# Kernel optimization log

Hardware: AMD Instinct MI355X
Metric: run time of the kernel (lower is better)

Reference implementation:

```python
import jax, jax.numpy as jnp
from jax import lax
import numpy as np

EPS = 1e-5
STRIDE = 4
K_NEIGHBORS = 16


def setup_inputs() -> dict:
    key = jax.random.key(0)
    ks = jax.random.split(key, 4)
    B, N, Cin, Cout = 16, 4096, 64, 128
    p1 = jax.random.normal(ks[0], (B, N, 3), dtype=jnp.float32)
    x1 = jax.random.normal(ks[1], (B, Cin, N), dtype=jnp.float32)
    w1 = jax.random.normal(ks[2], (Cout, Cin + 3), dtype=jnp.float32) * 0.05
    w2 = jax.random.normal(ks[3], (Cout, Cout), dtype=jnp.float32) * 0.05
    g1 = jnp.ones((Cout,), jnp.float32)
    b1 = jnp.zeros((Cout,), jnp.float32)
    g2 = jnp.ones((Cout,), jnp.float32)
    b2 = jnp.zeros((Cout,), jnp.float32)
    return {"p1": p1, "x1": x1, "w1": w1, "g1": g1, "b1": b1,
            "w2": w2, "g2": g2, "b2": b2}


def farthest_point_sampling(p, npoint):
    # p: [B, N, 3] -> centroids [B, npoint] (deterministic start at index 0)
    B, N, _ = p.shape
    gather_pt = jax.vmap(lambda pts, f: pts[f])  # [B,N,3],[B] -> [B,3]

    def step(carry, _):
        dist, farthest = carry
        centroid = gather_pt(p, farthest)                     # [B, 3]
        d = jnp.sum((p - centroid[:, None, :]) ** 2, -1)      # [B, N]
        dist = jnp.minimum(dist, d)
        new_far = jnp.argmax(dist, axis=-1).astype(jnp.int32)
        return (dist, new_far), farthest

    init = (jnp.full((B, N), 1e10, dtype=p.dtype), jnp.zeros((B,), jnp.int32))
    _, idxs = lax.scan(step, init, None, length=npoint)       # [npoint, B]
    return idxs.T                                             # [B, npoint]


def knn_point(k, xyz, new_xyz):
    # squared distances via gram trick; exclude all-zero points like the original
    n1 = jnp.sum(xyz ** 2, -1)                                # [B, N]
    n2 = jnp.sum(new_xyz ** 2, -1)                            # [B, M]
    d2 = n2[:, :, None] + n1[:, None, :] - 2.0 * jnp.einsum('bmc,bnc->bmn', new_xyz, xyz)
    zero_mask = jnp.all(xyz == 0, axis=-1)                    # [B, N]
    d2 = jnp.where(zero_mask[:, None, :], jnp.inf, d2)
    _, idx = lax.top_k(-d2, k)                                # smallest-k -> [B, M, k]
    return idx


def _bn_relu(h, g, b):
    # BatchNorm2d (training-mode batch stats, biased var) over (B, M, k) per channel
    m = jnp.mean(h, axis=(0, 1, 2), keepdims=True)
    v = jnp.mean((h - m) ** 2, axis=(0, 1, 2), keepdims=True)
    return jax.nn.relu(g * (h - m) * lax.rsqrt(v + EPS) + b)


def reference(p1, x1, w1, g1, b1, w2, g2, b2):
    B, N, _ = p1.shape
    M = max(1, N // STRIDE)
    k = K_NEIGHBORS

    idx = farthest_point_sampling(p1, M)                      # [B, M]
    gather2 = jax.vmap(lambda pts, i: pts[i])
    p2 = gather2(p1, idx)                                     # [B, M, 3]

    idx_knn = knn_point(k, p1, p2)                            # [B, M, k]
    grouped_p1 = gather2(p1, idx_knn)                         # [B, M, k, 3]
    xt = jnp.transpose(x1, (0, 2, 1))                         # [B, N, Cin]
    grouped_x1 = gather2(xt, idx_knn)                         # [B, M, k, Cin]

    rel = grouped_p1 - p2[:, :, None, :]                      # [B, M, k, 3]
    feats = jnp.concatenate([rel, grouped_x1], axis=-1)       # [B, M, k, 3+Cin]

    h = _bn_relu(jnp.einsum('bmkc,oc->bmko', feats, w1), g1, b1)
    h = _bn_relu(jnp.einsum('bmkc,oc->bmko', h, w2), g2, b2)
    new_features = jnp.max(h, axis=2)                         # maxpool over k -> [B, M, Cout]
    return p2, jnp.transpose(new_features, (0, 2, 1))         # ([B,M,3], [B,Cout,M])
```

## Files before the change

### kernel.cpp

```cpp
#include <hip/hip_runtime.h>
#include <hip/hip_bf16.h>
#include <hip/hip_cooperative_groups.h>
#include <cstdint>

namespace cg = cooperative_groups;

#define BB 16
#define NN 4096
#define MM 1024
#define KNB 16
#define CIN 64
#define COUT 128
#define RTOT (BB*MM*KNB)
#define AP1 104
#define AP2 136

typedef __attribute__((ext_vector_type(8))) short short8v;
typedef __attribute__((ext_vector_type(4))) float floatx4;
typedef __attribute__((ext_vector_type(2))) float f32x2;
typedef __attribute__((ext_vector_type(2))) unsigned int uint2v;

__device__ __forceinline__ float bflo(uint32_t u){ return __uint_as_float(u << 16); }
__device__ __forceinline__ float bfhi(uint32_t u){ return __uint_as_float(u & 0xffff0000u); }
__device__ __forceinline__ uint32_t f2bf_pk(float a, float b){
  uint32_t ua = __float_as_uint(a), ub = __float_as_uint(b);
  ua += 0x7fffu + ((ua >> 16) & 1u);
  ub += 0x7fffu + ((ub >> 16) & 1u);
  return (ua >> 16) | (ub & 0xffff0000u);
}
__device__ __forceinline__ uint16_t f2bf1(float a){
  uint32_t u = __float_as_uint(a);
  u += 0x7fffu + ((u >> 16) & 1u);
  return (uint16_t)(u >> 16);
}
template<int CTRL>
__device__ __forceinline__ float dpp_f(float v){
  return __int_as_float(__builtin_amdgcn_update_dpp(__float_as_int(v), __float_as_int(v), CTRL, 0xf, 0xf, false));
}
__device__ __forceinline__ float plmax16(float v){
#if __has_builtin(__builtin_amdgcn_permlane16_swap)
  uint2v r = __builtin_amdgcn_permlane16_swap(__float_as_uint(v), __float_as_uint(v), false, false);
  return fmaxf(__uint_as_float(r[0]), __uint_as_float(r[1]));
#else
  return fmaxf(v, __int_as_float(__builtin_amdgcn_ds_swizzle(__float_as_int(v), 0x401F)));
#endif
}
__device__ __forceinline__ float plmax32(float v){
#if __has_builtin(__builtin_amdgcn_permlane32_swap)
  uint2v r = __builtin_amdgcn_permlane32_swap(__float_as_uint(v), __float_as_uint(v), false, false);
  return fmaxf(__uint_as_float(r[0]), __uint_as_float(r[1]));
#else
  return fmaxf(v, __shfl_xor(v, 32));
#endif
}

struct FpsS { float4 pcv[NN]; float4 sel[MM]; unsigned long long candk[2][4]; };
struct TrS  { float t[64][65]; };
struct ConsS{ uint16_t Bh1[128*AP1]; uint16_t AhD[128*AP2];
              int winq[8*16]; float ssum[128]; float ssq[128]; };
union PreU  { FpsS fps; TrS tr; ConsS cons; };

__global__ __launch_bounds__(512, 2) void k_pre2(
    const float* __restrict__ p1, const float* __restrict__ x1,
    const float* __restrict__ w1,
    float* __restrict__ outp2, float* __restrict__ p2w,
    float4* __restrict__ p1n, uint16_t* __restrict__ xtb, float* __restrict__ Sz,
    uint16_t* __restrict__ h1, float* __restrict__ S1,
    int* __restrict__ prog, int* __restrict__ prep_done)
{
  __shared__ PreU u;
  const int blk = blockIdx.x, tid = threadIdx.x;
  const int lane = tid & 63, wid = tid >> 6;

  if (blk < 16){
    int b = blk;
    const float* pb = p1 + (size_t)b*NN*3;
    {
      float4 f[6];
      const float4* src = (const float4*)(pb + tid*24);
      #pragma unroll
      for (int j=0;j<6;j++) f[j] = src[j];
      const float* fa = (const float*)f;
      #pragma unroll
      for (int j=0;j<8;j++)
        u.fps.pcv[tid*8 + j] = make_float4(fa[3*j], fa[3*j+1], fa[3*j+2], 0.f);
    }
    __syncthreads();
    float4 c00 = u.fps.pcv[0];
    float cx = c00.x, cy = c00.y, cz = c00.z;
    if (tid==64) u.fps.sel[0] = make_float4(cx, cy, cz, 0.f);

    f32x2 px2[8] = {}, py2[8] = {}, pz2[8] = {}, ds2[8] = {};
    const int g0 = tid*16;
    if (wid < 4){
      #pragma unroll
      for (int j=0;j<8;j++){
        float4 a = u.fps.pcv[g0 + 2*j];
        float4 bq = u.fps.pcv[g0 + 2*j + 1];
        px2[j][0]=a.x; px2[j][1]=bq.x;
        py2[j][0]=a.y; py2[j][1]=bq.y;
        pz2[j][0]=a.z; pz2[j][1]=bq.z;
        ds2[j][0]=1e10f; ds2[j][1]=1e10f;
      }
    }

    for (int i=1;i<MM;i++){
      if (wid < 4){
        {
          #pragma clang fp contract(off)
          f32x2 cx2; cx2[0]=cx; cx2[1]=cx;
          f32x2 cy2; cy2[0]=cy; cy2[1]=cy;
          f32x2 cz2; cz2[0]=cz; cz2[1]=cz;
          #pragma unroll
          for (int j=0;j<8;j++){
            f32x2 dx = px2[j] - cx2;
            f32x2 dy = py2[j] - cy2;
            f32x2 dz = pz2[j] - cz2;
            f32x2 d  = dx*dx + dy*dy + dz*dz;
            ds2[j] = __builtin_elementwise_min(ds2[j], d);
          }
        }
        f32x2 t0 = __builtin_elementwise_max(ds2[0], ds2[1]);
        f32x2 t1 = __builtin_elementwise_max(ds2[2], ds2[3]);
        f32x2 t2 = __builtin_elementwise_max(ds2[4], ds2[5]);
        f32x2 t3 = __builtin_elementwise_max(ds2[6], ds2[7]);
        f32x2 u0 = __builtin_elementwise_max(t0, t1);
        f32x2 u1 = __builtin_elementwise_max(t2, t3);
        f32x2 vv = __builtin_elementwise_max(u0, u1);
        float lm = fmaxf(vv[0], vv[1]);
        int li = g0 + 15;
        #pragma unroll
        for (int j=14;j>=0;j--){
          float ev = ds2[j>>1][j & 1];
          li = (ev == lm) ? (g0 + j) : li;
        }
        float wm = lm;
        wm = fmaxf(wm, dpp_f<0xB1>(wm));
        wm = fmaxf(wm, dpp_f<0x4E>(wm));
        wm = fmaxf(wm, dpp_f<0x124>(wm));
        wm = fmaxf(wm, dpp_f<0x128>(wm));
        wm = plmax16(wm);
        wm = plmax32(wm);
        unsigned long long bmask = __ballot(lm == wm);
        int fl = __ffsll(bmask) - 1;
        int wi = __builtin_amdgcn_readlane(li, fl);
        if (lane == 0)
          u.fps.candk[i&1][wid] = (((unsigned long long)(unsigned)__float_as_uint(wm)) << 32)
                                   | (unsigned)(0xFFFFu ^ (unsigned)wi);
      }
      __syncthreads();
      if (wid < 4){
        const unsigned long long* cd = u.fps.candk[i&1];
        unsigned long long cq0=cd[0], cq1=cd[1], cq2=cd[2], cq3=cd[3];
        unsigned long long a0 = cq0>cq1?cq0:cq1, a1 = cq2>cq3?cq2:cq3;
        unsigned long long mb = a0>a1?a0:a1;
        int midx = (int)(0xFFFFu ^ (unsigned)(mb & 0xFFFFull));
        float4 cv = u.fps.pcv[midx];
        cx = cv.x; cy = cv.y; cz = cv.z;
        if (tid==64) u.fps.sel[i] = make_float4(cx, cy, cz, 0.f);
      } else if (wid == 4 && (i & 63) == 0){
        int e = i - 64 + lane;
        float4 s = u.fps.sel[e];
        float n2 = __fadd_rn(__fadd_rn(__fmul_rn(s.x,s.x),__fmul_rn(s.y,s.y)),__fmul_rn(s.z,s.z));
        *(float4*)(p2w + ((size_t)b*MM + e)*4) = make_float4(s.x, s.y, s.z, n2);
        if (lane == 0)
          __hip_atomic_store(&prog[b*16], i, __ATOMIC_RELEASE, __HIP_MEMORY_SCOPE_AGENT);
      }
    }
    __syncthreads();
    if (wid == 4){
      int e = 960 + lane;
      float4 s = u.fps.sel[e];
      float n2 = __fadd_rn(__fadd_rn(__fmul_rn(s.x,s.x),__fmul_rn(s.y,s.y)),__fmul_rn(s.z,s.z));
      *(float4*)(p2w + ((size_t)b*MM + e)*4) = make_float4(s.x, s.y, s.z, n2);
      if (lane == 0)
        __hip_atomic_store(&prog[b*16], MM, __ATOMIC_RELEASE, __HIP_MEMORY_SCOPE_AGENT);
    }
    for (int e = tid; e < MM; e += 512){
      float4 s = u.fps.sel[e];
      float* o = outp2 + ((size_t)b*MM + e)*3;
      o[0]=s.x; o[1]=s.y; o[2]=s.z;
    }
  } else {
    for (int i = (blk-16)*512 + tid; i < 16384; i += 240*512) Sz[i] = 0.f;
    for (int i = (blk-16)*512 + tid; i < BB*NN; i += 240*512){
      float x = p1[(size_t)i*3+0], y = p1[(size_t)i*3+1], z = p1[(size_t)i*3+2];
      float n = __fadd_rn(__fadd_rn(__fmul_rn(x,x),__fmul_rn(y,y)),__fmul_rn(z,z));
      p1n[i] = make_float4(x,y,z,n);
    }
    for (int tile = blk-16; tile < 1024; tile += 240){
      int b = tile >> 6, n0 = (tile & 63)*64;
      __syncthreads();
      int c = tid >> 3, q = tid & 7;
      const float* src = x1 + ((size_t)(b*64 + c))*NN + n0 + q*8;
      float4 f0 = *(const float4*)src, f1 = *(const float4*)(src+4);
      u.tr.t[c][q*8+0]=f0.x; u.tr.t[c][q*8+1]=f0.y; u.tr.t[c][q*8+2]=f0.z; u.tr.t[c][q*8+3]=f0.w;
      u.tr.t[c][q*8+4]=f1.x; u.tr.t[c][q*8+5]=f1.y; u.tr.t[c][q*8+6]=f1.z; u.tr.t[c][q*8+7]=f1.w;
      __syncthreads();
      int n = tid >> 3;
      uint32_t* dst = (uint32_t*)(xtb + ((size_t)(b*NN + n0 + n))*64 + q*8);
      #pragma unroll
      for (int j=0;j<4;j++)
        dst[j] = f2bf_pk(u.tr.t[q*8+2*j][n], u.tr.t[q*8+2*j+1][n]);
    }
    __threadfence();
    __syncthreads();
    if (tid == 0) atomicAdd(prep_done, 1);
    for (int e = tid; e < 128*96; e += 512){
      int o = e / 96, k = e - o*96;
      float v = (k < 64) ? w1[o*67 + 3 + k] : ((k < 67) ? w1[o*67 + (k-64)] : 0.f);
      u.cons.Bh1[o*AP1 + k] = f2bf1(v);
    }
    if (tid < 128){ u.cons.ssum[tid]=0.f; u.cons.ssq[tid]=0.f; }
    __syncthreads();
    {
      int pv = 0, sp = 0;
      if (lane == 0) pv = __hip_atomic_load(prep_done, __ATOMIC_ACQUIRE, __HIP_MEMORY_SCOPE_AGENT);
      pv = __shfl(pv, 0);
      while (pv < 240 && sp < (1<<16)){
        __builtin_amdgcn_s_sleep(64);
        if (lane == 0) pv = __hip_atomic_load(prep_done, __ATOMIC_ACQUIRE, __HIP_MEMORY_SCOPE_AGENT);
        pv = __shfl(pv, 0); sp++;
      }
    }
    int ml = lane & 15, quad = lane >> 4, seg = lane >> 4;
    int gw = (blk-16)*8 + wid;
    for (int qi = gw; qi < BB*MM; qi += 1920){
      int b = qi & 15, m = qi >> 4;
      int q2 = b*MM + m;
      {
        int pv = 0, sp = 0;
        if (lane == 0) pv = __hip_atomic_load(&prog[b*16], __ATOMIC_ACQUIRE, __HIP_MEMORY_SCOPE_AGENT);
        pv = __shfl(pv, 0);
        while (pv <= m && sp < (1<<16)){
          __builtin_amdgcn_s_sleep(64);
          if (lane == 0) pv = __hip_atomic_load(&prog[b*16], __ATOMIC_ACQUIRE, __HIP_MEMORY_SCOPE_AGENT);
          pv = __shfl(pv, 0); sp++;
        }
      }
      const float4 qv = *(const float4*)(p2w + (size_t)q2*4);
      const float4* pbn = p1n + (size_t)b*NN;
      float bd[16]; int bi[16];
      #pragma unroll
      for (int s=0;s<16;s++){ bd[s] = 1e30f; bi[s] = 0; }
      float wv = 1e30f; int wslot = 0;

      #define KPROC(T, PV) { \
        float dot = fmaf(qv.z, (PV).z, fmaf(qv.y, (PV).y, __fmul_rn(qv.x, (PV).x))); \
        float d2 = __fsub_rn(__fadd_rn(qv.w, (PV).w), __fmul_rn(2.0f, dot)); \
        if (d2 < wv){ \
          int c = (T)*64 + lane; \
          _Pragma("unroll") \
          for (int s=0;s<16;s++) if (s==wslot){ bd[s]=d2; bi[s]=c; } \
          wv = bd[0]; wslot = 0; \
          _Pragma("unroll") \
          for (int s=1;s<16;s++) if (bd[s] > wv){ wv = bd[s]; wslot = s; } \
        } }

      float4 cur = pbn[lane];
      for (int t=0;t<63;t++){
        float4 nx = pbn[(t+1)*64 + lane];
        KPROC(t, cur);
        cur = nx;
      }
      KPROC(63, cur);
      #undef KPROC

      float lv = bd[0]; int ls = 0;
      #pragma unroll
      for (int s=1;s<16;s++) if (bd[s] < lv){ lv = bd[s]; ls = s; }
      for (int r=0;r<16;r++){
        float rv = lv; int rl = lane;
        #pragma unroll
        for (int off=32; off>=1; off>>=1){
          float ov = __shfl_xor(rv, off); int ol = __shfl_xor(rl, off);
          if (ov < rv || (ov == rv && ol < rl)){ rv = ov; rl = ol; }
        }
        if (lane == rl){
          int idx = 0;
          #pragma unroll
          for (int s=0;s<16;s++) if (s==ls) idx = bi[s];
          u.cons.winq[wid*16 + r] = idx;
          #pragma unroll
          for (int s=0;s<16;s++) if (s==ls) bd[s] = 1e30f;
          lv = bd[0]; ls = 0;
          #pragma unroll
          for (int s=1;s<16;s++) if (bd[s] < lv){ lv = bd[s]; ls = s; }
        }
      }
      int n = u.cons.winq[wid*16 + ml];
      {
        const uint4* s4 = (const uint4*)(xtb + ((size_t)(b*NN + n))*64 + seg*16);
        uint4* d4 = (uint4*)(u.cons.AhD + (wid*16 + ml)*AP2 + seg*16);
        d4[0] = s4[0]; d4[1] = s4[1];
        if (seg == 0){
          const float* pp = p1 + ((size_t)(b*NN + n))*3;
          float rx = __fsub_rn(pp[0], qv.x);
          float ry = __fsub_rn(pp[1], qv.y);
          float rz = __fsub_rn(pp[2], qv.z);
          uint4* dr = (uint4*)(u.cons.AhD + (wid*16 + ml)*AP2 + 64);
          dr[0] = make_uint4(f2bf_pk(rx, ry), f2bf_pk(rz, 0.f), 0u, 0u);
          dr[1] = make_uint4(0u,0u,0u,0u);
          dr[2] = make_uint4(0u,0u,0u,0u);
          dr[3] = make_uint4(0u,0u,0u,0u);
        }
      }
      short8v af[3];
      #pragma unroll
      for (int kc=0;kc<3;kc++)
        af[kc] = *(const short8v*)(u.cons.AhD + (wid*16 + ml)*AP2 + kc*32 + quad*8);
      floatx4 acc[8];
      #pragma unroll
      for (int ct=0;ct<8;ct++) acc[ct] = (floatx4){0.f,0.f,0.f,0.f};
      #pragma unroll
      for (int ct=0;ct<8;ct++){
        #pragma unroll
        for (int kc=0;kc<3;kc++){
          short8v bf = *(const short8v*)(u.cons.Bh1 + (ct*16+ml)*AP1 + kc*32 + quad*8);
          acc[ct] = __builtin_amdgcn_mfma_f32_16x16x32_bf16(af[kc], bf, acc[ct], 0, 0, 0);
        }
      }
      float csum[8], csq[8];
      #pragma unroll
      for (int ct=0;ct<8;ct++){
        float a0=acc[ct][0], a1=acc[ct][1], a2=acc[ct][2], a3=acc[ct][3];
        float s = (a0+a1)+(a2+a3);
        float qq2 = (a0*a0+a1*a1)+(a2*a2+a3*a3);
        s += __shfl_xor(s,16);  s += __shfl_xor(s,32);
        qq2 += __shfl_xor(qq2,16); qq2 += __shfl_xor(qq2,32);
        csum[ct]=s; csq[ct]=qq2;
        #pragma unroll
        for (int r=0;r<4;r++)
          u.cons.AhD[(wid*16 + quad*4 + r)*AP2 + ct*16 + ml] = f2bf1(acc[ct][r]);
      }
      #pragma unroll
      for (int jj=0;jj<2;jj++){
        int ct = quad*2 + jj, col = ct*16 + ml;
        atomicAdd(&u.cons.ssum[col], csum[ct]);
        atomicAdd(&u.cons.ssq[col],  csq[ct]);
      }
      {
        const uint4* s4 = (const uint4*)(u.cons.AhD + (wid*16 + ml)*AP2 + seg*32);
        uint4* dst = (uint4*)(h1 + ((size_t)q2*16 + ml)*128 + seg*32);
        dst[0]=s4[0]; dst[1]=s4[1]; dst[2]=s4[2]; dst[3]=s4[3];
      }
    }
    __syncthreads();
    int cp = (blk & 31)*256;
    if (tid < 128){ atomicAdd(&S1[cp+tid], u.cons.ssum[tid]); atomicAdd(&S1[cp+128+tid], u.cons.ssq[tid]); }
  }
}

__global__ __launch_bounds__(256) void k_gemm2(const __hip_bfloat16* __restrict__ h1,
                                               const float* __restrict__ w2,
                                               const float* __restrict__ g1v, const float* __restrict__ b1v,
                                               const float* __restrict__ S1, float* __restrict__ S2,
                                               float* __restrict__ hmax, float* __restrict__ hmin){
  __shared__ __hip_bfloat16 Ah[64*AP2];
  __shared__ __hip_bfloat16 Bh[128*AP2];
  __shared__ float scb[128], shb[128], ssum[128], ssq[128];
  int tid = threadIdx.x;
  if (tid < 128){
    float s=0.f, q=0.f;
    for (int c=0;c<32;c++){ s += S1[c*256+tid]; q += S1[c*256+128+tid]; }
    float inv = 1.0f / (float)RTOT;
    float mean = s * inv;
    float var  = q * inv - mean*mean;
    float rs = 1.0f / sqrtf(var + 1e-5f);
    float scv = g1v[tid] * rs;
    scb[tid] = scv;
    shb[tid] = b1v[tid] - mean*scv;
    ssum[tid] = 0.f; ssq[tid] = 0.f;
  }
  {
    int o = tid >> 1, hf = tid & 1;
    const float4* wr = (const float4*)(w2 + (size_t)o*128 + hf*64);
    uint32_t* bd = (uint32_t*)(Bh + o*AP2 + hf*64);
    #pragma unroll
    for (int q=0;q<16;q++){
      float4 v = wr[q];
      bd[2*q]   = f2bf_pk(v.x, v.y);
      bd[2*q+1] = f2bf_pk(v.z, v.w);
    }
  }
  __syncthreads();
  int lane = tid & 63, wid = tid >> 6;
  int m0 = wid*16, ml = lane & 15, quad = lane >> 4;
  for (int tile = blockIdx.x; tile < 4096; tile += 768){
    int r0 = tile * 64;
    if (tile != (int)blockIdx.x) __syncthreads();
    {
      int row = tid >> 2, seg = tid & 3;
      const uint4* hp4 = (const uint4*)(h1 + ((size_t)(r0+row))*128 + seg*32);
      #pragma unroll
      for (int q=0;q<4;q++){
        uint4 u = hp4[q];
        int cg = seg*32 + q*8;
        uint32_t wv[4] = {u.x,u.y,u.z,u.w};
        uint32_t ov[4];
        #pragma unroll
        for (int t=0;t<4;t++){
          int c = cg + t*2;
          float a0 = fmaxf(fmaf(bflo(wv[t]), scb[c],   shb[c]),   0.f);
          float a1 = fmaxf(fmaf(bfhi(wv[t]), scb[c+1], shb[c+1]), 0.f);
          ov[t] = f2bf_pk(a0, a1);
        }
        *(uint4*)(Ah + row*AP2 + cg) = make_uint4(ov[0],ov[1],ov[2],ov[3]);
      }
    }
    __syncthreads();
    short8v af[4];
    #pragma unroll
    for (int kc=0;kc<4;kc++)
      af[kc] = *(const short8v*)(Ah + (m0+ml)*AP2 + kc*32 + quad*8);
    floatx4 acc[8];
    #pragma unroll
    for (int ct=0;ct<8;ct++) acc[ct] = (floatx4){0.f,0.f,0.f,0.f};
    #pragma unroll
    for (int ct=0;ct<8;ct++){
      #pragma unroll
      for (int kc=0;kc<4;kc++){
        short8v bf = *(const short8v*)(Bh + (ct*16+ml)*AP2 + kc*32 + quad*8);
        acc[ct] = __builtin_amdgcn_mfma_f32_16x16x32_bf16(af[kc], bf, acc[ct], 0, 0, 0);
      }
    }
    int mrow = (r0 >> 4) + wid;
    float cm[8], cn[8], cs[8], cq[8];
    #pragma unroll
    for (int ct=0;ct<8;ct++){
      float a0=acc[ct][0], a1=acc[ct][1], a2=acc[ct][2], a3=acc[ct][3];
      float mx = fmaxf(fmaxf(a0,a1), fmaxf(a2,a3));
      float mn = fminf(fminf(a0,a1), fminf(a2,a3));
      float s  = (a0+a1)+(a2+a3);
      float q2 = (a0*a0+a1*a1)+(a2*a2+a3*a3);
      mx = fmaxf(mx, __shfl_xor(mx,16)); mx = fmaxf(mx, __shfl_xor(mx,32));
      mn = fminf(mn, __shfl_xor(mn,16)); mn = fminf(mn, __shfl_xor(mn,32));
      s += __shfl_xor(s,16);  s += __shfl_xor(s,32);
      q2 += __shfl_xor(q2,16); q2 += __shfl_xor(q2,32);
      cm[ct]=mx; cn[ct]=mn; cs[ct]=s; cq[ct]=q2;
    }
    #pragma unroll
    for (int jj=0;jj<2;jj++){
      int ct = quad*2 + jj, col = ct*16 + ml;
      hmax[(size_t)mrow*128 + col] = cm[ct];
      hmin[(size_t)mrow*128 + col] = cn[ct];
      atomicAdd(&ssum[col], cs[ct]);
      atomicAdd(&ssq[col],  cq[ct]);
    }
  }
  __syncthreads();
  int cp = (blockIdx.x & 31)*256;
  if (tid < 128){ atomicAdd(&S2[cp+tid], ssum[tid]); atomicAdd(&S2[cp+128+tid], ssq[tid]); }
}

__global__ __launch_bounds__(256) void k_pool(const float* __restrict__ hmax, const float* __restrict__ hmin,
                                              const float* __restrict__ g2v, const float* __restrict__ b2v,
                                              const float* __restrict__ S2, float* __restrict__ out1){
  __shared__ float ot[128*65];
  __shared__ float scs[128], shs[128];
  int tid = threadIdx.x, blk = blockIdx.x;
  int b = blk >> 4, m0 = (blk & 15) * 64;
  if (tid < 128){
    float s=0.f, q=0.f;
    for (int c=0;c<32;c++){ s += S2[c*256+tid]; q += S2[c*256+128+tid]; }
    float inv = 1.0f / (float)RTOT;
    float mean = s * inv;
    float var  = q * inv - mean*mean;
    float rs = 1.0f / sqrtf(var + 1e-5f);
    float scv = g2v[tid] * rs;
    scs[tid] = scv;
    shs[tid] = b2v[tid] - mean*scv;
  }
  __syncthreads();
  int ml = tid >> 2, oq = tid & 3, o0 = oq*32;
  int gm = b*MM + m0 + ml;
  const float4* xr = (const float4*)(hmax + (size_t)gm*128 + o0);
  const float4* nr = (const float4*)(hmin + (size_t)gm*128 + o0);
  #pragma unroll
  for (int j2=0;j2<8;j2++){
    float4 hx = xr[j2], hn = nr[j2];
    float hv[4] = {hx.x, hx.y, hx.z, hx.w};
    float nv[4] = {hn.x, hn.y, hn.z, hn.w};
    #pragma unroll
    for (int e=0;e<4;e++){
      int c = o0 + j2*4 + e;
      float sc = scs[c], sh = shs[c];
      float h = (sc >= 0.f) ? hv[e] : nv[e];
      ot[c*65 + ml] = fmaxf(fmaf(h, sc, sh), 0.f);
    }
  }
  __syncthreads();
  int o = tid >> 1, mh = tid & 1;
  float* dst = out1 + ((size_t)(b*COUT + o))*MM + m0 + mh*32;
  #pragma unroll
  for (int j2=0;j2<8;j2++){
    float4 v;
    v.x=ot[o*65+mh*32+j2*4+0]; v.y=ot[o*65+mh*32+j2*4+1];
    v.z=ot[o*65+mh*32+j2*4+2]; v.w=ot[o*65+mh*32+j2*4+3];
    *(float4*)(dst + j2*4) = v;
  }
}

extern "C" void kernel_launch(void* const* d_in, const int* in_sizes, int n_in,
                              void* d_out, int out_size, void* d_ws, size_t ws_size,
                              hipStream_t stream) {
  (void)in_sizes; (void)n_in; (void)out_size; (void)ws_size;
  const float* p1 = (const float*)d_in[0];
  const float* x1 = (const float*)d_in[1];
  const float* w1 = (const float*)d_in[2];
  const float* g1 = (const float*)d_in[3];
  const float* b1 = (const float*)d_in[4];
  const float* w2 = (const float*)d_in[5];
  const float* g2 = (const float*)d_in[6];
  const float* b2 = (const float*)d_in[7];
  float* out = (float*)d_out;
  float* ws  = (float*)d_ws;

  uint16_t* xtb = (uint16_t*)ws;
  float4* p1n   = (float4*)(ws + 2097152);
  float*  p2w   = ws + 2621440;
  float*  S1    = ws + 2686976;
  float*  S2    = ws + 2695168;
  uint16_t* h1  = (uint16_t*)(ws + 2703872);
  float*  hmax  = ws + 19481088;
  float*  hmin  = ws + 21578240;
  int*    prog  = (int*)(ws + 23675392);
  int*    prep_done = (int*)(ws + 23675392) + 256;
  float*  outp2 = out;
  float*  out1  = out + 49152;

  hipMemsetAsync(prog, 0, 2048, stream);

  k_pre2<<<256, 512, 0, stream>>>(p1, x1, w1, outp2, p2w, p1n, xtb, S1,
                                  h1, S1, prog, prep_done);

  k_gemm2<<<768, 256, 0, stream>>>((const __hip_bfloat16*)h1, w2, g1, b1, S1, S2, hmax, hmin);
  k_pool<<<256, 256, 0, stream>>>(hmax, hmin, g2, b2, S2, out1);
}
```

Measured before the change: 832.2 us.

## Fuse pooling kernel into gemm2 via global atomic completion counter

Merges the final BN2+ReLU+maxpool kernel into the second GEMM kernel. Each block increments a global done counter after publishing its BN statistics, and the first 256 blocks spin-wait until all 768 blocks finish before doing the pooling and transpose. Shared memory is unioned between the GEMM tiles and the pooling staging buffer. This removes one kernel launch and its boundary, but depends on all 768 blocks being co-resident or otherwise scheduled to completion. Waiting blocks also hold CUs while they spin.

```diff
diff --git a/kernel.cpp b/kernel.cpp
--- a/kernel.cpp
+++ b/kernel.cpp
@@ -351,13 +351,16 @@
   }
 }
 
-__global__ __launch_bounds__(256) void k_gemm2(const __hip_bfloat16* __restrict__ h1,
-                                               const float* __restrict__ w2,
-                                               const float* __restrict__ g1v, const float* __restrict__ b1v,
-                                               const float* __restrict__ S1, float* __restrict__ S2,
-                                               float* __restrict__ hmax, float* __restrict__ hmin){
-  __shared__ __hip_bfloat16 Ah[64*AP2];
-  __shared__ __hip_bfloat16 Bh[128*AP2];
+union G2U { struct { __hip_bfloat16 Ah[64*AP2]; __hip_bfloat16 Bh[128*AP2]; } g;
+            struct { float ot[128*65]; float scs[128]; float shs[128]; } p; };
+__global__ __launch_bounds__(256) void k_gemm2f(const __hip_bfloat16* __restrict__ h1,
+                                                const float* __restrict__ w2,
+                                                const float* __restrict__ g1v, const float* __restrict__ b1v,
+                                                const float* __restrict__ S1, float* __restrict__ S2,
+                                                const float* __restrict__ g2v, const float* __restrict__ b2v,
+                                                float* __restrict__ hmax, float* __restrict__ hmin,
+                                                float* __restrict__ out1, int* __restrict__ done2){
+  __shared__ G2U su;
   __shared__ float scb[128], shb[128], ssum[128], ssq[128];
   int tid = threadIdx.x;
   if (tid < 128){
@@ -375,7 +378,7 @@
   {
     int o = tid >> 1, hf = tid & 1;
     const float4* wr = (const float4*)(w2 + (size_t)o*128 + hf*64);
-    uint32_t* bd = (uint32_t*)(Bh + o*AP2 + hf*64);
+    uint32_t* bd = (uint32_t*)(su.g.Bh + o*AP2 + hf*64);
     #pragma unroll
     for (int q=0;q<16;q++){
       float4 v = wr[q];
@@ -405,14 +408,14 @@
           float a1 = fmaxf(fmaf(bfhi(wv[t]), scb[c+1], shb[c+1]), 0.f);
           ov[t] = f2bf_pk(a0, a1);
         }
-        *(uint4*)(Ah + row*AP2 + cg) = make_uint4(ov[0],ov[1],ov[2],ov[3]);
+        *(uint4*)(su.g.Ah + row*AP2 + cg) = make_uint4(ov[0],ov[1],ov[2],ov[3]);
       }
     }
     __syncthreads();
     short8v af[4];
     #pragma unroll
     for (int kc=0;kc<4;kc++)
-      af[kc] = *(const short8v*)(Ah + (m0+ml)*AP2 + kc*32 + quad*8);
+      af[kc] = *(const short8v*)(su.g.Ah + (m0+ml)*AP2 + kc*32 + quad*8);
     floatx4 acc[8];
     #pragma unroll
     for (int ct=0;ct<8;ct++) acc[ct] = (floatx4){0.f,0.f,0.f,0.f};
@@ -420,7 +423,7 @@
     for (int ct=0;ct<8;ct++){
       #pragma unroll
       for (int kc=0;kc<4;kc++){
-        short8v bf = *(const short8v*)(Bh + (ct*16+ml)*AP2 + kc*32 + quad*8);
+        short8v bf = *(const short8v*)(su.g.Bh + (ct*16+ml)*AP2 + kc*32 + quad*8);
         acc[ct] = __builtin_amdgcn_mfma_f32_16x16x32_bf16(af[kc], bf, acc[ct], 0, 0, 0);
       }
     }
@@ -449,55 +452,68 @@
     }
   }
   __syncthreads();
-  int cp = (blockIdx.x & 31)*256;
-  if (tid < 128){ atomicAdd(&S2[cp+tid], ssum[tid]); atomicAdd(&S2[cp+128+tid], ssq[tid]); }
-}
-
-__global__ __launch_bounds__(256) void k_pool(const float* __restrict__ hmax, const float* __restrict__ hmin,
-                                              const float* __restrict__ g2v, const float* __restrict__ b2v,
-                                              const float* __restrict__ S2, float* __restrict__ out1){
-  __shared__ float ot[128*65];
-  __shared__ float scs[128], shs[128];
-  int tid = threadIdx.x, blk = blockIdx.x;
-  int b = blk >> 4, m0 = (blk & 15) * 64;
-  if (tid < 128){
-    float s=0.f, q=0.f;
-    for (int c=0;c<32;c++){ s += S2[c*256+tid]; q += S2[c*256+128+tid]; }
-    float inv = 1.0f / (float)RTOT;
-    float mean = s * inv;
-    float var  = q * inv - mean*mean;
-    float rs = 1.0f / sqrtf(var + 1e-5f);
-    float scv = g2v[tid] * rs;
-    scs[tid] = scv;
-    shs[tid] = b2v[tid] - mean*scv;
-  }
+  {
+    int cp = (blockIdx.x & 31)*256;
+    if (tid < 128){ atomicAdd(&S2[cp+tid], ssum[tid]); atomicAdd(&S2[cp+128+tid], ssq[tid]); }
+  }
+  __threadfence();
   __syncthreads();
-  int ml = tid >> 2, oq = tid & 3, o0 = oq*32;
-  int gm = b*MM + m0 + ml;
-  const float4* xr = (const float4*)(hmax + (size_t)gm*128 + o0);
-  const float4* nr = (const float4*)(hmin + (size_t)gm*128 + o0);
-  #pragma unroll
-  for (int j2=0;j2<8;j2++){
-    float4 hx = xr[j2], hn = nr[j2];
-    float hv[4] = {hx.x, hx.y, hx.z, hx.w};
-    float nv[4] = {hn.x, hn.y, hn.z, hn.w};
-    #pragma unroll
-    for (int e=0;e<4;e++){
-      int c = o0 + j2*4 + e;
-      float sc = scs[c], sh = shs[c];
-      float h = (sc >= 0.f) ? hv[e] : nv[e];
-      ot[c*65 + ml] = fmaxf(fmaf(h, sc, sh), 0.f);
-    }
-  }
-  __syncthreads();
-  int o = tid >> 1, mh = tid & 1;
-  float* dst = out1 + ((size_t)(b*COUT + o))*MM + m0 + mh*32;
-  #pragma unroll
-  for (int j2=0;j2<8;j2++){
-    float4 v;
-    v.x=ot[o*65+mh*32+j2*4+0]; v.y=ot[o*65+mh*32+j2*4+1];
-    v.z=ot[o*65+mh*32+j2*4+2]; v.w=ot[o*65+mh*32+j2*4+3];
-    *(float4*)(dst + j2*4) = v;
+  if (tid == 0) __hip_atomic_fetch_add(done2, 1, __ATOMIC_ACQ_REL, __HIP_MEMORY_SCOPE_AGENT);
+  if (blockIdx.x >= 256) return;
+  {
+    int sp = 0;
+    if (tid == 0){
+      int dv;
+      do {
+        dv = __hip_atomic_load(done2, __ATOMIC_ACQUIRE, __HIP_MEMORY_SCOPE_AGENT);
+        if (dv >= 768) break;
+        __builtin_amdgcn_s_sleep(32);
+      } while (++sp < (1<<22));
+    }
+    __syncthreads();
+  }
+  {
+    int blk = blockIdx.x;
+    int b = blk >> 4, pm0 = (blk & 15) * 64;
+    if (tid < 128){
+      float s=0.f, q=0.f;
+      for (int c=0;c<32;c++){ s += S2[c*256+tid]; q += S2[c*256+128+tid]; }
+      float inv = 1.0f / (float)RTOT;
+      float mean = s * inv;
+      float var  = q * inv - mean*mean;
+      float rs = 1.0f / sqrtf(var + 1e-5f);
+      float scv = g2v[tid] * rs;
+      su.p.scs[tid] = scv;
+      su.p.shs[tid] = b2v[tid] - mean*scv;
+    }
+    __syncthreads();
+    int pml = tid >> 2, oq = tid & 3, o0 = oq*32;
+    int gm = b*MM + pm0 + pml;
+    const float4* xr = (const float4*)(hmax + (size_t)gm*128 + o0);
+    const float4* nr = (const float4*)(hmin + (size_t)gm*128 + o0);
+    #pragma unroll
+    for (int j2=0;j2<8;j2++){
+      float4 hx = xr[j2], hn = nr[j2];
+      float hv[4] = {hx.x, hx.y, hx.z, hx.w};
+      float nv[4] = {hn.x, hn.y, hn.z, hn.w};
+      #pragma unroll
+      for (int e=0;e<4;e++){
+        int c = o0 + j2*4 + e;
+        float sc = su.p.scs[c], sh = su.p.shs[c];
+        float h = (sc >= 0.f) ? hv[e] : nv[e];
+        su.p.ot[c*65 + pml] = fmaxf(fmaf(h, sc, sh), 0.f);
+      }
+    }
+    __syncthreads();
+    int o = tid >> 1, mh = tid & 1;
+    float* dst = out1 + ((size_t)(b*COUT + o))*MM + pm0 + mh*32;
+    #pragma unroll
+    for (int j2=0;j2<8;j2++){
+      float4 v;
+      v.x=su.p.ot[o*65+mh*32+j2*4+0]; v.y=su.p.ot[o*65+mh*32+j2*4+1];
+      v.z=su.p.ot[o*65+mh*32+j2*4+2]; v.w=su.p.ot[o*65+mh*32+j2*4+3];
+      *(float4*)(dst + j2*4) = v;
+    }
   }
 }
 
@@ -526,6 +542,7 @@
   float*  hmin  = ws + 21578240;
   int*    prog  = (int*)(ws + 23675392);
   int*    prep_done = (int*)(ws + 23675392) + 256;
+  int*    done2 = (int*)(ws + 23675392) + 257;
   float*  outp2 = out;
   float*  out1  = out + 49152;
 
@@ -534,6 +551,6 @@
   k_pre2<<<256, 512, 0, stream>>>(p1, x1, w1, outp2, p2w, p1n, xtb, S1,
                                   h1, S1, prog, prep_done);
 
-  k_gemm2<<<768, 256, 0, stream>>>((const __hip_bfloat16*)h1, w2, g1, b1, S1, S2, hmax, hmin);
-  k_pool<<<256, 256, 0, stream>>>(hmax, hmin, g2, b2, S2, out1);
-}
+  k_gemm2f<<<768, 256, 0, stream>>>((const __hip_bfloat16*)h1, w2, g1, b1, S1, S2,
+                                    g2, b2, hmax, hmin, out1, done2);
+}
```

Result: slower. 943.7 us (+13.4%).
